# Performance work log

Hardware: AMD Instinct MI355X
Metric: run time of the kernel (lower is better)

The kernel has to match this reference:

```python
import jax, jax.numpy as jnp
import numpy as np
from jax import lax


def setup_inputs() -> dict:
    key = jax.random.key(0)
    ks = jax.random.split(key, 8)
    V, E, H = 128, 256, 512
    B, S = 128, 2048
    return {
        "x": jax.random.randint(ks[0], (B, S), 0, V),
        "emb": jax.random.normal(ks[1], (V, E), jnp.float32) * 0.02,
        "Wx": jax.random.normal(ks[2], (E, H), jnp.float32) * 0.02,
        "bx": jnp.zeros((H,), jnp.float32),
        "Wh": jax.random.normal(ks[3], (H, H), jnp.float32) * 0.02,
        "bh": jnp.zeros((H,), jnp.float32),
        "Wfc": jax.random.normal(ks[4], (H, V), jnp.float32) * 0.02,
        "bfc": jnp.zeros((V,), jnp.float32),
    }


def reference(x, emb, Wx, bx, Wh, bh, Wfc, bfc):
    # x: [B, S] int token ids
    B, S = x.shape
    H = Wh.shape[0]
    xe = emb[x]  # [B, S, E]
    # Precompute input projection for all timesteps (batched GEMM)
    xw = jnp.einsum('bse,eh->bsh', xe, Wx) + bx  # [B, S, H]

    def step(h, xt):  # xt: [B, H]
        h = jnp.tanh(xt + h @ Wh + bh)
        return h, h

    h0 = jnp.zeros((B, H), xw.dtype)
    _, hs = lax.scan(step, h0, jnp.swapaxes(xw, 0, 1))  # hs: [S, B, H]
    out = jnp.einsum('sbh,hv->bsv', hs, Wfc) + bfc  # [B, S, V]
    return out
```

## Files before the change

### kernel.cpp

```cpp
#include <hip/hip_runtime.h>
#include <hip/hip_fp16.h>

typedef _Float16 h16;
typedef _Float16 half8 __attribute__((ext_vector_type(8)));
typedef _Float16 half4v __attribute__((ext_vector_type(4)));
typedef float f32x4 __attribute__((ext_vector_type(4)));
typedef unsigned long long u64;

#define NB 128
#define NS 2048
#define NH 512
#define NV 128
#define NE 256

#define WS_M2    0
#define WS_WHT   (256*1024)
#define WS_WFCT  (768*1024)
#define WS_EXCH  (896*1024)
#define WS_FLAG  (1152*1024)

__device__ __forceinline__ float tanh_fast(float v) {
  float e = __expf(2.0f * v);
  return 1.0f - __fdividef(2.0f, e + 1.0f);
}

__global__ void vrnn_prep(const float* __restrict__ emb, const float* __restrict__ Wx,
                          const float* __restrict__ bx, const float* __restrict__ Wh,
                          const float* __restrict__ bh, const float* __restrict__ Wfc,
                          unsigned char* __restrict__ ws) {
  float* M2 = (float*)(ws + WS_M2);
  h16* WhT = (h16*)(ws + WS_WHT);
  h16* WfcT = (h16*)(ws + WS_WFCT);
  int* flags = (int*)(ws + WS_FLAG);
  const int bid = blockIdx.x, tid = threadIdx.x;
  if (bid < 128) {
    __shared__ float le[NE];
    le[tid] = emb[bid*NE + tid];
    __syncthreads();
    for (int hh = 0; hh < 2; ++hh) {
      int n = tid + hh*256;
      float s = bx[n] + bh[n];
      for (int e = 0; e < NE; ++e) s = fmaf(le[e], Wx[e*NH + n], s);
      M2[bid*NH + n] = s;
    }
  } else if (bid < 192) {
    const int base = (bid - 128)*4096;
    for (int i = 0; i < 16; ++i) {
      int idx = base + i*256 + tid;
      WhT[(idx & 511)*NH + (idx >> 9)] = (h16)Wh[idx];
    }
  } else if (bid < 208) {
    const int base = (bid - 192)*4096;
    for (int i = 0; i < 16; ++i) {
      int idx = base + i*256 + tid;
      WfcT[(idx & 127)*NH + (idx >> 7)] = (h16)Wfc[idx];
    }
  } else {
    flags[tid] = 0;
  }
}

__global__ void __launch_bounds__(256, 1)
vrnn_scan(const int* __restrict__ x, const float* __restrict__ bfc,
          float* __restrict__ out, unsigned char* __restrict__ ws) {
  const float* M2 = (const float*)(ws + WS_M2);
  const h16* WhT = (const h16*)(ws + WS_WHT);
  const h16* WfcT = (const h16*)(ws + WS_WFCT);
  h16* exch = (h16*)(ws + WS_EXCH);
  int* flags = (int*)(ws + WS_FLAG);

  const int bid = blockIdx.x;
  const int side = bid >> 3;
  const int c = bid & 7;
  const int rowbase = c*16;
  const int tid = threadIdx.x;
  const int w = tid >> 6;
  const int l = tid & 63;
  const int m = l & 15;
  const int g = l >> 4;
  const int swz = (m & 7) << 3;

  const int n0w = side*256 + w*64;
  const int v0w = side*64 + w*16;
  const int ksOwn = side*8;
  const int ksPar = (1 - side)*8;

  __shared__ h16 hlds[2][16][NH];

  for (int i = tid; i < 16*NH/4; i += 256) ((u64*)&hlds[0][0][0])[i] = 0ull;

  half8 whf[4][16];
  half8 wfcf[16];
#pragma unroll
  for (int j = 0; j < 16; ++j) {
    const int ks = (j < 8) ? (ksOwn + j) : (ksPar + j - 8);
#pragma unroll
    for (int nt = 0; nt < 4; ++nt)
      whf[nt][j] = *(const half8*)&WhT[(n0w + nt*16 + m)*NH + ks*32 + g*8];
    wfcf[j] = *(const half8*)&WfcT[(v0w + m)*NH + ks*32 + g*8];
  }

  const f32x4 bfcf = *(const f32x4*)&bfc[v0w + g*4];

  int* flag_own = flags + (c*2 + side)*16;
  int* flag_par = flags + (c*2 + (1 - side))*16;

  const int* xrow = x + (rowbase + m)*NS;
  f32x4 ubuf[4];
  {
    const int tok0 = xrow[0];
#pragma unroll
    for (int nt = 0; nt < 4; ++nt)
      ubuf[nt] = *(const f32x4*)&M2[tok0*NH + n0w + nt*16 + g*4];
  }
  int tok_n = xrow[1];

  __syncthreads();

  for (int t = 0; t < NS; ++t) {
    const int p = t & 1;

    f32x4 acc[4];
#pragma unroll
    for (int nt = 0; nt < 4; ++nt) acc[nt] = ubuf[nt];
    f32x4 oacc = bfcf;

    const int tok_use = tok_n;
    tok_n = xrow[(t + 2 < NS) ? (t + 2) : (NS - 1)];
#pragma unroll
    for (int nt = 0; nt < 4; ++nt)
      ubuf[nt] = *(const f32x4*)&M2[tok_use*NH + n0w + nt*16 + g*4];

    {
      half8 bfr[8];
#pragma unroll
      for (int i = 0; i < 8; ++i)
        bfr[i] = *(const half8*)&hlds[p][m][(((ksOwn + i)*32) + g*8) ^ swz];
#pragma unroll
      for (int i = 0; i < 8; ++i) {
#pragma unroll
        for (int nt = 0; nt < 4; ++nt)
          acc[nt] = __builtin_amdgcn_mfma_f32_16x16x32_f16(whf[nt][i], bfr[i], acc[nt], 0, 0, 0);
        oacc = __builtin_amdgcn_mfma_f32_16x16x32_f16(wfcf[i], bfr[i], oacc, 0, 0, 0);
      }
    }

    if (t > 0) {
      while (__hip_atomic_load(flag_par, __ATOMIC_ACQUIRE, __HIP_MEMORY_SCOPE_AGENT) < t)
        __builtin_amdgcn_s_sleep(1);
      const h16* src = exch + ((c*2 + ((t - 1) & 1))*2 + (1 - side))*4096;
      const int mm = w*4 + g;
      const int nch = (l & 15)*16;
      u64* sp = (u64*)&src[mm*256 + nch];
      const u64 d0 = __hip_atomic_load(sp + 0, __ATOMIC_RELAXED, __HIP_MEMORY_SCOPE_AGENT);
      const u64 d1 = __hip_atomic_load(sp + 1, __ATOMIC_RELAXED, __HIP_MEMORY_SCOPE_AGENT);
      const u64 d2 = __hip_atomic_load(sp + 2, __ATOMIC_RELAXED, __HIP_MEMORY_SCOPE_AGENT);
      const u64 d3 = __hip_atomic_load(sp + 3, __ATOMIC_RELAXED, __HIP_MEMORY_SCOPE_AGENT);
      const int swzm = (mm & 7) << 3;
      const int pk = (1 - side)*256 + nch;
      u64* q0 = (u64*)&hlds[p][mm][(pk) ^ swzm];
      u64* q1 = (u64*)&hlds[p][mm][(pk + 8) ^ swzm];
      q0[0] = d0; q0[1] = d1;
      q1[0] = d2; q1[1] = d3;
    }
    __syncthreads();

    {
      half8 bfr[8];
#pragma unroll
      for (int i = 0; i < 8; ++i)
        bfr[i] = *(const half8*)&hlds[p][m][(((ksPar + i)*32) + g*8) ^ swz];
#pragma unroll
      for (int i = 0; i < 8; ++i) {
#pragma unroll
        for (int nt = 0; nt < 4; ++nt)
          acc[nt] = __builtin_amdgcn_mfma_f32_16x16x32_f16(whf[nt][8 + i], bfr[i], acc[nt], 0, 0, 0);
        oacc = __builtin_amdgcn_mfma_f32_16x16x32_f16(wfcf[8 + i], bfr[i], oacc, 0, 0, 0);
      }
    }

    if (t > 0) {
      float* po = out + ((size_t)(rowbase + m)*NS + (t - 1))*NV + v0w + g*4;
      *(f32x4*)po = oacc;
    }

    {
      const int pn = p ^ 1;
      h16* exo = exch + ((c*2 + p)*2 + side)*4096;
#pragma unroll
      for (int nt = 0; nt < 4; ++nt) {
        const f32x4 a = acc[nt];
        half4v hv;
#pragma unroll
        for (int r = 0; r < 4; ++r) hv[r] = (h16)tanh_fast(a[r]);
        const int kb = n0w + nt*16 + g*4;
        *(half4v*)&hlds[pn][m][kb ^ swz] = hv;
        union { half4v v; u64 u; } cv; cv.v = hv;
        __hip_atomic_store((u64*)&exo[m*256 + (w*64 + nt*16 + g*4)], cv.u,
                           __ATOMIC_RELAXED, __HIP_MEMORY_SCOPE_AGENT);
      }
    }
    __syncthreads();
    if (tid == 0)
      __hip_atomic_store(flag_own, t + 1, __ATOMIC_RELEASE, __HIP_MEMORY_SCOPE_AGENT);
  }

  {
    f32x4 oacc = bfcf;
    {
      half8 bfr[8];
#pragma unroll
      for (int i = 0; i < 8; ++i)
        bfr[i] = *(const half8*)&hlds[0][m][(((ksOwn + i)*32) + g*8) ^ swz];
#pragma unroll
      for (int i = 0; i < 8; ++i)
        oacc = __builtin_amdgcn_mfma_f32_16x16x32_f16(wfcf[i], bfr[i], oacc, 0, 0, 0);
    }
    while (__hip_atomic_load(flag_par, __ATOMIC_ACQUIRE, __HIP_MEMORY_SCOPE_AGENT) < NS)
      __builtin_amdgcn_s_sleep(1);
    {
      const h16* src = exch + ((c*2 + 1)*2 + (1 - side))*4096;
      const int mm = w*4 + g;
      const int nch = (l & 15)*16;
      u64* sp = (u64*)&src[mm*256 + nch];
      const u64 d0 = __hip_atomic_load(sp + 0, __ATOMIC_RELAXED, __HIP_MEMORY_SCOPE_AGENT);
      const u64 d1 = __hip_atomic_load(sp + 1, __ATOMIC_RELAXED, __HIP_MEMORY_SCOPE_AGENT);
      const u64 d2 = __hip_atomic_load(sp + 2, __ATOMIC_RELAXED, __HIP_MEMORY_SCOPE_AGENT);
      const u64 d3 = __hip_atomic_load(sp + 3, __ATOMIC_RELAXED, __HIP_MEMORY_SCOPE_AGENT);
      const int swzm = (mm & 7) << 3;
      const int pk = (1 - side)*256 + nch;
      u64* q0 = (u64*)&hlds[0][mm][(pk) ^ swzm];
      u64* q1 = (u64*)&hlds[0][mm][(pk + 8) ^ swzm];
      q0[0] = d0; q0[1] = d1;
      q1[0] = d2; q1[1] = d3;
    }
    __syncthreads();
    {
      half8 bfr[8];
#pragma unroll
      for (int i = 0; i < 8; ++i)
        bfr[i] = *(const half8*)&hlds[0][m][(((ksPar + i)*32) + g*8) ^ swz];
#pragma unroll
      for (int i = 0; i < 8; ++i)
        oacc = __builtin_amdgcn_mfma_f32_16x16x32_f16(wfcf[8 + i], bfr[i], oacc, 0, 0, 0);
    }
    float* po = out + ((size_t)(rowbase + m)*NS + (NS - 1))*NV + v0w + g*4;
    *(f32x4*)po = oacc;
  }
}

extern "C" void kernel_launch(void* const* d_in, const int* in_sizes, int n_in,
                              void* d_out, int out_size, void* d_ws, size_t ws_size,
                              hipStream_t stream) {
  (void)in_sizes; (void)n_in; (void)out_size; (void)ws_size;
  const int*   x   = (const int*)d_in[0];
  const float* emb = (const float*)d_in[1];
  const float* Wx  = (const float*)d_in[2];
  const float* bx  = (const float*)d_in[3];
  const float* Wh  = (const float*)d_in[4];
  const float* bh  = (const float*)d_in[5];
  const float* Wfc = (const float*)d_in[6];
  const float* bfc = (const float*)d_in[7];
  float* out = (float*)d_out;
  unsigned char* ws = (unsigned char*)d_ws;

  hipLaunchKernelGGL(vrnn_prep, dim3(209), dim3(256), 0, stream,
                     emb, Wx, bx, Wh, bh, Wfc, ws);
  hipLaunchKernelGGL(vrnn_scan, dim3(16), dim3(256), 0, stream,
                     x, bfc, out, ws);
}
```

Before: 6.191 ms.

## Interleave two batch row-groups per block to hide cross-block exchange latency

Each of the 8 blocks now owns two 16-row batch groups (X and Y) instead of one, halving the grid. Each group's step is computed while the partner block's exchange for the other group is in flight, so the flag wait and the global loads overlap with useful MFMA work. Weight fragments are pinned in AGPRs via inline asm constraints, and the input projection is added after the matmul rather than used as the initial accumulator. This trades per-block parallelism (fewer CUs used, twice the serial work per block) for hiding the synchronisation latency that dominates each timestep.

New measurement: 14.14 ms. +128.4%, slower.

```diff
diff --git a/kernel.cpp b/kernel.cpp
--- a/kernel.cpp
+++ b/kernel.cpp
@@ -7,7 +7,6 @@
 typedef float f32x4 __attribute__((ext_vector_type(4)));
 typedef unsigned long long u64;
 
-#define NB 128
 #define NS 2048
 #define NH 512
 #define NV 128
@@ -57,8 +56,38 @@
     }
   } else {
     flags[tid] = 0;
+    flags[tid + 256] = 0;
   }
 }
+
+#define COMPUTE16(CI, BUF)                                                     \
+  {                                                                            \
+    half8 bfr[8];                                                              \
+    _Pragma("unroll")                                                          \
+    for (int i = 0; i < 8; ++i)                                                \
+      bfr[i] = *(const half8*)&hlds[CI][BUF][m][((i*32) + g*8) ^ swz];         \
+    _Pragma("unroll")                                                          \
+    for (int i = 0; i < 8; ++i) {                                              \
+      _Pragma("unroll")                                                        \
+      for (int nt = 0; nt < 4; ++nt)                                           \
+        acc[nt] = __builtin_amdgcn_mfma_f32_16x16x32_f16(                      \
+            __builtin_bit_cast(half8, whf[nt][i]), bfr[i], acc[nt], 0, 0, 0);  \
+      oacc = __builtin_amdgcn_mfma_f32_16x16x32_f16(                           \
+          __builtin_bit_cast(half8, wfcf[i]), bfr[i], oacc, 0, 0, 0);          \
+    }                                                                          \
+    _Pragma("unroll")                                                          \
+    for (int i = 0; i < 8; ++i)                                                \
+      bfr[i] = *(const half8*)&hlds[CI][BUF][m][(((i+8)*32) + g*8) ^ swz];     \
+    _Pragma("unroll")                                                          \
+    for (int i = 0; i < 8; ++i) {                                              \
+      _Pragma("unroll")                                                        \
+      for (int nt = 0; nt < 4; ++nt)                                           \
+        acc[nt] = __builtin_amdgcn_mfma_f32_16x16x32_f16(                      \
+            __builtin_bit_cast(half8, whf[nt][8+i]), bfr[i], acc[nt], 0, 0, 0);\
+      oacc = __builtin_amdgcn_mfma_f32_16x16x32_f16(                           \
+          __builtin_bit_cast(half8, wfcf[8+i]), bfr[i], oacc, 0, 0, 0);        \
+    }                                                                          \
+  }
 
 __global__ void __launch_bounds__(256, 1)
 vrnn_scan(const int* __restrict__ x, const float* __restrict__ bfc,
@@ -70,183 +99,213 @@
   int* flags = (int*)(ws + WS_FLAG);
 
   const int bid = blockIdx.x;
-  const int side = bid >> 3;
-  const int c = bid & 7;
-  const int rowbase = c*16;
+  const int pair = bid & 3;
+  const int side = bid >> 2;
+  const int rowX = pair * 32;
+  const int rowY = rowX + 16;
   const int tid = threadIdx.x;
   const int w = tid >> 6;
   const int l = tid & 63;
   const int m = l & 15;
   const int g = l >> 4;
   const int swz = (m & 7) << 3;
+  const int mm = w*4 + g;
+  const int swzm = (mm & 7) << 3;
+  const int pk = (1 - side)*256 + m*16;
 
   const int n0w = side*256 + w*64;
   const int v0w = side*64 + w*16;
-  const int ksOwn = side*8;
-  const int ksPar = (1 - side)*8;
-
-  __shared__ h16 hlds[2][16][NH];
-
-  for (int i = tid; i < 16*NH/4; i += 256) ((u64*)&hlds[0][0][0])[i] = 0ull;
-
-  half8 whf[4][16];
-  half8 wfcf[16];
-#pragma unroll
-  for (int j = 0; j < 16; ++j) {
-    const int ks = (j < 8) ? (ksOwn + j) : (ksPar + j - 8);
+
+  __shared__ h16 hlds[2][2][16][NH];
+
+  { u64* z = (u64*)&hlds[0][0][0][0];
+#pragma unroll
+    for (int i = 0; i < 32; ++i) z[tid + i*256] = 0ull; }
+
+  f32x4 whf[4][16];
+  f32x4 wfcf[16];
+#pragma unroll
+  for (int ks = 0; ks < 16; ++ks) {
 #pragma unroll
     for (int nt = 0; nt < 4; ++nt)
-      whf[nt][j] = *(const half8*)&WhT[(n0w + nt*16 + m)*NH + ks*32 + g*8];
-    wfcf[j] = *(const half8*)&WfcT[(v0w + m)*NH + ks*32 + g*8];
+      whf[nt][ks] = *(const f32x4*)&WhT[(n0w + nt*16 + m)*NH + ks*32 + g*8];
+    wfcf[ks] = *(const f32x4*)&WfcT[(v0w + m)*NH + ks*32 + g*8];
+  }
+#pragma unroll
+  for (int ks = 0; ks < 16; ++ks) {
+#pragma unroll
+    for (int nt = 0; nt < 4; ++nt)
+      asm volatile("" : "+a"(whf[nt][ks]));
+    asm volatile("" : "+a"(wfcf[ks]));
   }
 
   const f32x4 bfcf = *(const f32x4*)&bfc[v0w + g*4];
 
-  int* flag_own = flags + (c*2 + side)*16;
-  int* flag_par = flags + (c*2 + (1 - side))*16;
-
-  const int* xrow = x + (rowbase + m)*NS;
-  f32x4 ubuf[4];
-  {
-    const int tok0 = xrow[0];
-#pragma unroll
-    for (int nt = 0; nt < 4; ++nt)
-      ubuf[nt] = *(const f32x4*)&M2[tok0*NH + n0w + nt*16 + g*4];
-  }
-  int tok_n = xrow[1];
+  int* fXown = flags + ((pair*2 + 0)*2 + side)*32;
+  int* fXpar = flags + ((pair*2 + 0)*2 + (1 - side))*32;
+  int* fYown = flags + ((pair*2 + 1)*2 + side)*32;
+  int* fYpar = flags + ((pair*2 + 1)*2 + (1 - side))*32;
+
+  h16*       exoX = exch + (((pair*2 + 0)*2 + 0)*2 + side)*4096;
+  const h16* exiX = exch + (((pair*2 + 0)*2 + 0)*2 + (1 - side))*4096;
+  h16*       exoY = exch + (((pair*2 + 1)*2 + 0)*2 + side)*4096;
+  const h16* exiY = exch + (((pair*2 + 1)*2 + 0)*2 + (1 - side))*4096;
+
+  const int* xrowX = x + (rowX + m)*NS;
+  const int* xrowY = x + (rowY + m)*NS;
+  int tokX = xrowX[0], tokY = xrowY[0];
+
+  u64 dX0=0, dX1=0, dX2=0, dX3=0;
+  u64 dY0=0, dY1=0, dY2=0, dY3=0;
 
   __syncthreads();
 
   for (int t = 0; t < NS; ++t) {
-    const int p = t & 1;
-
-    f32x4 acc[4];
-#pragma unroll
-    for (int nt = 0; nt < 4; ++nt) acc[nt] = ubuf[nt];
-    f32x4 oacc = bfcf;
-
-    const int tok_use = tok_n;
-    tok_n = xrow[(t + 2 < NS) ? (t + 2) : (NS - 1)];
-#pragma unroll
-    for (int nt = 0; nt < 4; ++nt)
-      ubuf[nt] = *(const f32x4*)&M2[tok_use*NH + n0w + nt*16 + g*4];
+    const int p = t & 1, pn = p ^ 1;
+    const int tnext = (t + 1 < NS) ? (t + 1) : (NS - 1);
 
     {
-      half8 bfr[8];
-#pragma unroll
-      for (int i = 0; i < 8; ++i)
-        bfr[i] = *(const half8*)&hlds[p][m][(((ksOwn + i)*32) + g*8) ^ swz];
-#pragma unroll
-      for (int i = 0; i < 8; ++i) {
-#pragma unroll
-        for (int nt = 0; nt < 4; ++nt)
-          acc[nt] = __builtin_amdgcn_mfma_f32_16x16x32_f16(whf[nt][i], bfr[i], acc[nt], 0, 0, 0);
-        oacc = __builtin_amdgcn_mfma_f32_16x16x32_f16(wfcf[i], bfr[i], oacc, 0, 0, 0);
-      }
-    }
-
-    if (t > 0) {
-      while (__hip_atomic_load(flag_par, __ATOMIC_ACQUIRE, __HIP_MEMORY_SCOPE_AGENT) < t)
-        __builtin_amdgcn_s_sleep(1);
-      const h16* src = exch + ((c*2 + ((t - 1) & 1))*2 + (1 - side))*4096;
-      const int mm = w*4 + g;
-      const int nch = (l & 15)*16;
-      u64* sp = (u64*)&src[mm*256 + nch];
-      const u64 d0 = __hip_atomic_load(sp + 0, __ATOMIC_RELAXED, __HIP_MEMORY_SCOPE_AGENT);
-      const u64 d1 = __hip_atomic_load(sp + 1, __ATOMIC_RELAXED, __HIP_MEMORY_SCOPE_AGENT);
-      const u64 d2 = __hip_atomic_load(sp + 2, __ATOMIC_RELAXED, __HIP_MEMORY_SCOPE_AGENT);
-      const u64 d3 = __hip_atomic_load(sp + 3, __ATOMIC_RELAXED, __HIP_MEMORY_SCOPE_AGENT);
-      const int swzm = (mm & 7) << 3;
-      const int pk = (1 - side)*256 + nch;
-      u64* q0 = (u64*)&hlds[p][mm][(pk) ^ swzm];
-      u64* q1 = (u64*)&hlds[p][mm][(pk + 8) ^ swzm];
-      q0[0] = d0; q0[1] = d1;
-      q1[0] = d2; q1[1] = d3;
-    }
-    __syncthreads();
-
-    {
-      half8 bfr[8];
-#pragma unroll
-      for (int i = 0; i < 8; ++i)
-        bfr[i] = *(const half8*)&hlds[p][m][(((ksPar + i)*32) + g*8) ^ swz];
-#pragma unroll
-      for (int i = 0; i < 8; ++i) {
-#pragma unroll
-        for (int nt = 0; nt < 4; ++nt)
-          acc[nt] = __builtin_amdgcn_mfma_f32_16x16x32_f16(whf[nt][8 + i], bfr[i], acc[nt], 0, 0, 0);
-        oacc = __builtin_amdgcn_mfma_f32_16x16x32_f16(wfcf[8 + i], bfr[i], oacc, 0, 0, 0);
-      }
-    }
-
-    if (t > 0) {
-      float* po = out + ((size_t)(rowbase + m)*NS + (t - 1))*NV + v0w + g*4;
-      *(f32x4*)po = oacc;
-    }
-
-    {
-      const int pn = p ^ 1;
-      h16* exo = exch + ((c*2 + p)*2 + side)*4096;
+      f32x4 uf[4];
+#pragma unroll
+      for (int nt = 0; nt < 4; ++nt)
+        uf[nt] = *(const f32x4*)&M2[tokX*NH + n0w + nt*16 + g*4];
+      tokX = xrowX[tnext];
+
+      f32x4 acc[4];
+#pragma unroll
+      for (int nt = 0; nt < 4; ++nt) acc[nt] = f32x4{0.f,0.f,0.f,0.f};
+      f32x4 oacc = bfcf;
+
+      COMPUTE16(0, p)
+
+      if (t > 0) {
+        float* po = out + ((size_t)(rowX + m)*NS + (t - 1))*NV + v0w + g*4;
+        *(f32x4*)po = oacc;
+      }
+
+      h16* exo = exoX + p*8192;
 #pragma unroll
       for (int nt = 0; nt < 4; ++nt) {
         const f32x4 a = acc[nt];
         half4v hv;
 #pragma unroll
-        for (int r = 0; r < 4; ++r) hv[r] = (h16)tanh_fast(a[r]);
+        for (int r = 0; r < 4; ++r) hv[r] = (h16)tanh_fast(a[r] + uf[nt][r]);
         const int kb = n0w + nt*16 + g*4;
-        *(half4v*)&hlds[pn][m][kb ^ swz] = hv;
+        *(half4v*)&hlds[0][pn][m][kb ^ swz] = hv;
         union { half4v v; u64 u; } cv; cv.v = hv;
         __hip_atomic_store((u64*)&exo[m*256 + (w*64 + nt*16 + g*4)], cv.u,
                            __ATOMIC_RELAXED, __HIP_MEMORY_SCOPE_AGENT);
       }
-    }
-    __syncthreads();
-    if (tid == 0)
-      __hip_atomic_store(flag_own, t + 1, __ATOMIC_RELEASE, __HIP_MEMORY_SCOPE_AGENT);
+
+      if (t > 0) {
+        u64* q0 = (u64*)&hlds[1][p][mm][(pk) ^ swzm];
+        u64* q1 = (u64*)&hlds[1][p][mm][(pk + 8) ^ swzm];
+        q0[0] = dY0; q0[1] = dY1; q1[0] = dY2; q1[1] = dY3;
+      }
+
+      int fX = __hip_atomic_load(fXpar, __ATOMIC_ACQUIRE, __HIP_MEMORY_SCOPE_AGENT);
+      __syncthreads();
+      if (tid == 0)
+        __hip_atomic_store(fXown, t + 1, __ATOMIC_RELEASE, __HIP_MEMORY_SCOPE_AGENT);
+      while (fX < t + 1) {
+        __builtin_amdgcn_s_sleep(1);
+        fX = __hip_atomic_load(fXpar, __ATOMIC_ACQUIRE, __HIP_MEMORY_SCOPE_AGENT);
+      }
+      {
+        const u64* sp = (const u64*)&exiX[p*8192 + mm*256 + m*16];
+        dX0 = __hip_atomic_load(sp + 0, __ATOMIC_RELAXED, __HIP_MEMORY_SCOPE_AGENT);
+        dX1 = __hip_atomic_load(sp + 1, __ATOMIC_RELAXED, __HIP_MEMORY_SCOPE_AGENT);
+        dX2 = __hip_atomic_load(sp + 2, __ATOMIC_RELAXED, __HIP_MEMORY_SCOPE_AGENT);
+        dX3 = __hip_atomic_load(sp + 3, __ATOMIC_RELAXED, __HIP_MEMORY_SCOPE_AGENT);
+      }
+    }
+
+    {
+      f32x4 uf[4];
+#pragma unroll
+      for (int nt = 0; nt < 4; ++nt)
+        uf[nt] = *(const f32x4*)&M2[tokY*NH + n0w + nt*16 + g*4];
+      tokY = xrowY[tnext];
+
+      f32x4 acc[4];
+#pragma unroll
+      for (int nt = 0; nt < 4; ++nt) acc[nt] = f32x4{0.f,0.f,0.f,0.f};
+      f32x4 oacc = bfcf;
+
+      COMPUTE16(1, p)
+
+      if (t > 0) {
+        float* po = out + ((size_t)(rowY + m)*NS + (t - 1))*NV + v0w + g*4;
+        *(f32x4*)po = oacc;
+      }
+
+      h16* exo = exoY + p*8192;
+#pragma unroll
+      for (int nt = 0; nt < 4; ++nt) {
+        const f32x4 a = acc[nt];
+        half4v hv;
+#pragma unroll
+        for (int r = 0; r < 4; ++r) hv[r] = (h16)tanh_fast(a[r] + uf[nt][r]);
+        const int kb = n0w + nt*16 + g*4;
+        *(half4v*)&hlds[1][pn][m][kb ^ swz] = hv;
+        union { half4v v; u64 u; } cv; cv.v = hv;
+        __hip_atomic_store((u64*)&exo[m*256 + (w*64 + nt*16 + g*4)], cv.u,
+                           __ATOMIC_RELAXED, __HIP_MEMORY_SCOPE_AGENT);
+      }
+
+      {
+        u64* q0 = (u64*)&hlds[0][pn][mm][(pk) ^ swzm];
+        u64* q1 = (u64*)&hlds[0][pn][mm][(pk + 8) ^ swzm];
+        q0[0] = dX0; q0[1] = dX1; q1[0] = dX2; q1[1] = dX3;
+      }
+
+      int fY = __hip_atomic_load(fYpar, __ATOMIC_ACQUIRE, __HIP_MEMORY_SCOPE_AGENT);
+      __syncthreads();
+      if (tid == 0)
+        __hip_atomic_store(fYown, t + 1, __ATOMIC_RELEASE, __HIP_MEMORY_SCOPE_AGENT);
+      while (fY < t + 1) {
+        __builtin_amdgcn_s_sleep(1);
+        fY = __hip_atomic_load(fYpar, __ATOMIC_ACQUIRE, __HIP_MEMORY_SCOPE_AGENT);
+      }
+      {
+        const u64* sp = (const u64*)&exiY[p*8192 + mm*256 + m*16];
+        dY0 = __hip_atomic_load(sp + 0, __ATOMIC_RELAXED, __HIP_MEMORY_SCOPE_AGENT);
+        dY1 = __hip_atomic_load(sp + 1, __ATOMIC_RELAXED, __HIP_MEMORY_SCOPE_AGENT);
+        dY2 = __hip_atomic_load(sp + 2, __ATOMIC_RELAXED, __HIP_MEMORY_SCOPE_AGENT);
+        dY3 = __hip_atomic_load(sp + 3, __ATOMIC_RELAXED, __HIP_MEMORY_SCOPE_AGENT);
+      }
+    }
   }
 
   {
-    f32x4 oacc = bfcf;
-    {
-      half8 bfr[8];
-#pragma unroll
-      for (int i = 0; i < 8; ++i)
-        bfr[i] = *(const half8*)&hlds[0][m][(((ksOwn + i)*32) + g*8) ^ swz];
-#pragma unroll
-      for (int i = 0; i < 8; ++i)
-        oacc = __builtin_amdgcn_mfma_f32_16x16x32_f16(wfcf[i], bfr[i], oacc, 0, 0, 0);
-    }
-    while (__hip_atomic_load(flag_par, __ATOMIC_ACQUIRE, __HIP_MEMORY_SCOPE_AGENT) < NS)
-      __builtin_amdgcn_s_sleep(1);
-    {
-      const h16* src = exch + ((c*2 + 1)*2 + (1 - side))*4096;
-      const int mm = w*4 + g;
-      const int nch = (l & 15)*16;
-      u64* sp = (u64*)&src[mm*256 + nch];
-      const u64 d0 = __hip_atomic_load(sp + 0, __ATOMIC_RELAXED, __HIP_MEMORY_SCOPE_AGENT);
-      const u64 d1 = __hip_atomic_load(sp + 1, __ATOMIC_RELAXED, __HIP_MEMORY_SCOPE_AGENT);
-      const u64 d2 = __hip_atomic_load(sp + 2, __ATOMIC_RELAXED, __HIP_MEMORY_SCOPE_AGENT);
-      const u64 d3 = __hip_atomic_load(sp + 3, __ATOMIC_RELAXED, __HIP_MEMORY_SCOPE_AGENT);
-      const int swzm = (mm & 7) << 3;
-      const int pk = (1 - side)*256 + nch;
-      u64* q0 = (u64*)&hlds[0][mm][(pk) ^ swzm];
-      u64* q1 = (u64*)&hlds[0][mm][(pk + 8) ^ swzm];
-      q0[0] = d0; q0[1] = d1;
-      q1[0] = d2; q1[1] = d3;
-    }
-    __syncthreads();
-    {
-      half8 bfr[8];
-#pragma unroll
-      for (int i = 0; i < 8; ++i)
-        bfr[i] = *(const half8*)&hlds[0][m][(((ksPar + i)*32) + g*8) ^ swz];
-#pragma unroll
-      for (int i = 0; i < 8; ++i)
-        oacc = __builtin_amdgcn_mfma_f32_16x16x32_f16(wfcf[8 + i], bfr[i], oacc, 0, 0, 0);
-    }
-    float* po = out + ((size_t)(rowbase + m)*NS + (NS - 1))*NV + v0w + g*4;
-    *(f32x4*)po = oacc;
-  }
+    u64* q0 = (u64*)&hlds[1][0][mm][(pk) ^ swzm];
+    u64* q1 = (u64*)&hlds[1][0][mm][(pk + 8) ^ swzm];
+    q0[0] = dY0; q0[1] = dY1; q1[0] = dY2; q1[1] = dY3;
+  }
+  __syncthreads();
+#define TAILOUT(CI, TROW)                                                      \
+  {                                                                            \
+    f32x4 oacc = bfcf;                                                         \
+    half8 bfr[8];                                                              \
+    _Pragma("unroll")                                                          \
+    for (int i = 0; i < 8; ++i)                                                \
+      bfr[i] = *(const half8*)&hlds[CI][0][m][((i*32) + g*8) ^ swz];           \
+    _Pragma("unroll")                                                          \
+    for (int i = 0; i < 8; ++i)                                                \
+      oacc = __builtin_amdgcn_mfma_f32_16x16x32_f16(                           \
+          __builtin_bit_cast(half8, wfcf[i]), bfr[i], oacc, 0, 0, 0);          \
+    _Pragma("unroll")                                                          \
+    for (int i = 0; i < 8; ++i)                                                \
+      bfr[i] = *(const half8*)&hlds[CI][0][m][(((i+8)*32) + g*8) ^ swz];       \
+    _Pragma("unroll")                                                          \
+    for (int i = 0; i < 8; ++i)                                                \
+      oacc = __builtin_amdgcn_mfma_f32_16x16x32_f16(                           \
+          __builtin_bit_cast(half8, wfcf[8+i]), bfr[i], oacc, 0, 0, 0);        \
+    float* po = out + ((size_t)(TROW + m)*NS + (NS - 1))*NV + v0w + g*4;       \
+    *(f32x4*)po = oacc;                                                        \
+  }
+  TAILOUT(0, rowX)
+  TAILOUT(1, rowY)
 }
 
 extern "C" void kernel_launch(void* const* d_in, const int* in_sizes, int n_in,
@@ -266,6 +325,6 @@
 
   hipLaunchKernelGGL(vrnn_prep, dim3(209), dim3(256), 0, stream,
                      emb, Wx, bx, Wh, bh, Wfc, ws);
-  hipLaunchKernelGGL(vrnn_scan, dim3(16), dim3(256), 0, stream,
+  hipLaunchKernelGGL(vrnn_scan, dim3(8), dim3(256), 0, stream,
                      x, bfc, out, ws);
 }
```
